# Optimization experiments

Hardware: AMD Instinct MI355X
Metric: run time of the kernel (lower is better)

## Reference

```python
import itertools
import jax, jax.numpy as jnp
import numpy as np

B, N, D = 128, 1024, 256
G, GSZ, REL_DIM, KD, PD, NF = 64, 3, 16, 64, 64, 64


def sinusoidal_pe(n, d):
    # standard transformer sinusoidal positional encoding, shape (n, d)
    pos = jnp.arange(n, dtype=jnp.float32)[:, None]
    i = jnp.arange(d, dtype=jnp.float32)[None, :]
    angle = pos / jnp.power(10000.0, (2.0 * jnp.floor(i / 2.0)) / d)
    return jnp.where(jnp.arange(d)[None, :] % 2 == 0, jnp.sin(angle), jnp.cos(angle))


def setup_inputs() -> dict:
    key = jax.random.key(0)
    k0, k1, k2, k3, k4, k5 = jax.random.split(key, 6)
    x = jax.random.normal(k0, (B, N, D), jnp.float32)
    # graphlet filter bank (random_normal init)
    filters = 0.05 * jax.random.normal(k1, (NF, GSZ, GSZ, REL_DIM), jnp.float32)
    # learned group queries: Embedding(n_groups*graphlet_size, key_dim)
    query_emb = 0.05 * jax.random.normal(k2, (G * GSZ, KD), jnp.float32)
    # Dense(key_dim, use_bias=False) for attention keys
    Wk_map = jax.random.normal(k3, (D, KD), jnp.float32) / np.sqrt(D)
    # MultiDimInnerProdRelation: per-relation-dim query/key projections
    Wq = jax.random.normal(k4, (REL_DIM, D, PD), jnp.float32) / np.sqrt(D)
    Wk = jax.random.normal(k5, (REL_DIM, D, PD), jnp.float32) / np.sqrt(D)
    return {"x": x, "filters": filters, "query_emb": query_emb,
            "Wk_map": Wk_map, "Wq": Wq, "Wk": Wk}


def reference(x, filters, query_emb, Wk_map, Wq, Wk):
    beta = KD ** (-0.5)
    # group attention: keys = Dense(x) + positional embedding ('pos+feat')
    k = jnp.einsum('bnd,dk->bnk', x, Wk_map) + sinusoidal_pe(N, KD)[None]
    scores = jax.nn.softmax(beta * jnp.einsum('qk,bnk->bqn', query_emb, k), axis=-1)
    gobj = jnp.einsum('bqn,bnd->bqd', scores, x).reshape(B, G, GSZ, D)
    # MultiDimInnerProdRelation within each group: R[b,g,i,j,r] = <Wq_r x_i, Wk_r x_j>
    zq = jnp.einsum('bgnd,rdp->bgrnp', gobj, Wq)
    zk = jnp.einsum('bgmd,rdp->bgrmp', gobj, Wk)
    R = jnp.einsum('bgrnp,bgrmp->bgnmr', zq, zk)  # (B, G, GSZ, GSZ, REL_DIM)
    # symmetric relational inner product: aggregate (mean) over permutations
    perms = jnp.array(list(itertools.permutations(range(GSZ))))  # (P, GSZ)
    Rp = R[:, :, perms[:, :, None], perms[:, None, :], :]  # (B, G, P, GSZ, GSZ, REL_DIM)
    ip = jnp.einsum('bgpnmr,fnmr->bgpf', Rp, filters)
    return jnp.mean(ip, axis=2)  # (B, n_groups, n_filters)
```

## Files before the change

kernel.cpp:

```cpp
#include <hip/hip_runtime.h>
#include <math.h>

#define B_   128
#define N_   1024
#define D_   256
#define G_   64
#define GSZ_ 3
#define RD_  16
#define KD_  64
#define PD_  64
#define NF_  64
#define Q_   (G_*GSZ_)

typedef __attribute__((ext_vector_type(8))) short bf16x8;
typedef __attribute__((ext_vector_type(4))) float f32x4;

__device__ __forceinline__ unsigned short f2bf(float f) {
    unsigned int u = __float_as_uint(f);
    u += 0x7fffu + ((u >> 16) & 1u);
    return (unsigned short)(u >> 16);
}

__global__ void coef_kernel(const float* __restrict__ filters,
                            float* __restrict__ coef) {
    int flat = blockIdx.x * 256 + threadIdx.x;
    if (flat >= NF_ * RD_) return;
    int f = flat >> 4, r = flat & 15;
    const float* F = filters + f * 144 + r;
    float diag = F[0] + F[48 + 16] + F[96 + 32];
    float all = 0.f;
#pragma unroll
    for (int u = 0; u < 3; ++u)
#pragma unroll
        for (int v = 0; v < 3; ++v) all += F[u * 48 + v * 16];
    float a = diag * (1.f / 3.f);
    float b = (all - diag) * (1.f / 6.f);
    coef[f * 16 + r] = a - b;
    coef[1024 + f * 16 + r] = b;
}

__global__ void wb_kernel(const float* __restrict__ Wq,
                          const float* __restrict__ Wk,
                          unsigned short* __restrict__ Wb) {
    int flat = blockIdx.x * 256 + threadIdx.x;
    int d = flat & 255, col = flat >> 8;
    int ch = col & 1023;
    const float* W = (col >> 10) ? Wk : Wq;
    float v = W[((size_t)(ch >> 6) * 256 + d) * 64 + (ch & 63)];
    Wb[(size_t)col * 256 + d] = f2bf(v);
}

__global__ void qeb_kernel(const float* __restrict__ qe,
                           unsigned short* __restrict__ qeb) {
    int i = blockIdx.x * 256 + threadIdx.x;
    if (i < Q_ * KD_) qeb[i] = f2bf(qe[i] * 0.125f);
}

__global__ void wkt_kernel(const float* __restrict__ Wk_map,
                           unsigned short* __restrict__ WkTb) {
    int i = blockIdx.x * 256 + threadIdx.x;
    int kd = i >> 8, d = i & 255;
    WkTb[kd * 256 + d] = f2bf(Wk_map[d * 64 + kd]);
}

__global__ __launch_bounds__(256)
void xt_kernel(const float* __restrict__ x,
               unsigned short* __restrict__ xTb) {
    __shared__ float xs[128][65];
    int b = blockIdx.z, d0 = blockIdx.y * 64, n0 = blockIdx.x * 128;
    int t = threadIdx.x;
#pragma unroll
    for (int i = 0; i < 8; ++i) {
        int f = i * 256 + t;
        int row = f >> 4, c4 = f & 15;
        float4 v = *(const float4*)(x + ((size_t)b * N_ + n0 + row) * D_ + d0 + c4 * 4);
        xs[row][c4 * 4 + 0] = v.x; xs[row][c4 * 4 + 1] = v.y;
        xs[row][c4 * 4 + 2] = v.z; xs[row][c4 * 4 + 3] = v.w;
    }
    __syncthreads();
#pragma unroll
    for (int i = 0; i < 4; ++i) {
        int f = i * 256 + t;
        int dr = f >> 4, seg = f & 15;
        uint4 uv;
        unsigned int* up = (unsigned int*)&uv;
#pragma unroll
        for (int j = 0; j < 4; ++j) {
            unsigned int lo = f2bf(xs[seg * 8 + 2 * j][dr]);
            unsigned int hi = f2bf(xs[seg * 8 + 2 * j + 1][dr]);
            up[j] = lo | (hi << 16);
        }
        *(uint4*)(xTb + ((size_t)b * D_ + d0 + dr) * N_ + n0 + seg * 8) = uv;
    }
}

#define WKP 264

__global__ __launch_bounds__(256, 2)
void kproj2_kernel(const float* __restrict__ x,
                   const unsigned short* __restrict__ WkTb,
                   unsigned short* __restrict__ kb) {
    __shared__ unsigned short wkts[64 * WKP];
    __shared__ unsigned short xs[64 * WKP];
    __shared__ unsigned short Ks[64 * 72];
    int b = blockIdx.y, n0 = blockIdx.x * 64;
    int t = threadIdx.x, w = t >> 6, lane = t & 63;
    int quad = lane >> 4, lcol = lane & 15;

#pragma unroll
    for (int i = 0; i < 8; ++i) {
        int f = i * 256 + t;
        int row = f >> 5, seg = f & 31;
        *(uint4*)(&wkts[row * WKP + seg * 8]) = *(const uint4*)(WkTb + row * 256 + seg * 8);
    }
#pragma unroll
    for (int i = 0; i < 16; ++i) {
        int f = i * 256 + t;
        int row = f >> 6, c4 = f & 63;
        float4 v = *(const float4*)(x + ((size_t)b * N_ + n0 + row) * D_ + c4 * 4);
        uint2 uv;
        uv.x = (unsigned int)f2bf(v.x) | ((unsigned int)f2bf(v.y) << 16);
        uv.y = (unsigned int)f2bf(v.z) | ((unsigned int)f2bf(v.w) << 16);
        *(uint2*)(&xs[row * WKP + c4 * 4]) = uv;
    }
    __syncthreads();

    f32x4 z[4];
#pragma unroll
    for (int mt = 0; mt < 4; ++mt) z[mt] = (f32x4)(0.f);
#pragma unroll
    for (int kk = 0; kk < 8; ++kk) {
        bf16x8 bf = *(const bf16x8*)(&xs[(w * 16 + lcol) * WKP + kk * 32 + quad * 8]);
#pragma unroll
        for (int mt = 0; mt < 4; ++mt) {
            bf16x8 af = *(const bf16x8*)(&wkts[(mt * 16 + lcol) * WKP + kk * 32 + quad * 8]);
            z[mt] = __builtin_amdgcn_mfma_f32_16x16x32_bf16(af, bf, z[mt], 0, 0, 0);
        }
    }

    int nl = w * 16 + lcol;
    int n = n0 + nl;
#pragma unroll
    for (int mt = 0; mt < 4; ++mt)
#pragma unroll
        for (int r = 0; r < 4; ++r) {
            int kd = mt * 16 + quad * 4 + r;
            float freq  = expf(-(float)(kd >> 1) * (logf(10000.0f) / 32.0f));
            float angle = (float)n * freq;
            float pe    = (kd & 1) ? cosf(angle) : sinf(angle);
            Ks[nl * 72 + kd] = f2bf(z[mt][r] + pe);
        }
    __syncthreads();

#pragma unroll
    for (int i = 0; i < 2; ++i) {
        int f = i * 256 + t;
        int row = f >> 3, seg = f & 7;
        *(uint4*)(kb + ((size_t)b * N_ + n0 + row) * KD_ + seg * 8) =
            *(const uint4*)(&Ks[row * 72 + seg * 8]);
    }
}

#define KBP 72
#define XTP 72
#define PSP 72

__global__ __launch_bounds__(256, 2)
void attn2_kernel(const unsigned short* __restrict__ qeb,
                  const unsigned short* __restrict__ kb,
                  const unsigned short* __restrict__ xTb,
                  unsigned short* __restrict__ gobj) {
    __shared__ unsigned short kbs[64 * KBP];
    __shared__ unsigned short xts[256 * XTP];
    __shared__ unsigned short ps [96 * PSP];
    __shared__ float Rs[96][4];
    __shared__ float invs[96];

    int b = blockIdx.x >> 1, qh = blockIdx.x & 1;
    int t = threadIdx.x, w = t >> 6, lane = t & 63;
    int quad = lane >> 4, lcol = lane & 15;
    int q0 = qh * 96;

    bf16x8 qef[6][2];
#pragma unroll
    for (int mt = 0; mt < 6; ++mt)
#pragma unroll
        for (int ks = 0; ks < 2; ++ks)
            qef[mt][ks] = *(const bf16x8*)(qeb + (q0 + mt * 16 + lcol) * KD_ + ks * 32 + quad * 8);

    f32x4 acc[4][6];
#pragma unroll
    for (int i = 0; i < 4; ++i)
#pragma unroll
        for (int mt = 0; mt < 6; ++mt) acc[i][mt] = (f32x4)(0.f);
    float rsum[6][4];
#pragma unroll
    for (int mt = 0; mt < 6; ++mt)
#pragma unroll
        for (int r = 0; r < 4; ++r) rsum[mt][r] = 0.f;

    const unsigned short* kbB = kb + (size_t)b * N_ * KD_;
    const unsigned short* xtB = xTb + (size_t)b * D_ * N_;

    for (int c = 0; c < 16; ++c) {
        __syncthreads();
#pragma unroll
        for (int i = 0; i < 2; ++i) {
            int flat = i * 256 + t;
            int row = flat >> 3, seg = flat & 7;
            *(uint4*)(kbs + row * KBP + seg * 8) =
                *(const uint4*)(kbB + (size_t)(c * 64 + row) * KD_ + seg * 8);
        }
#pragma unroll
        for (int i = 0; i < 8; ++i) {
            int flat = i * 256 + t;
            int row = flat >> 3, seg = flat & 7;
            *(uint4*)(xts + row * XTP + seg * 8) =
                *(const uint4*)(xtB + (size_t)row * N_ + c * 64 + seg * 8);
        }
        __syncthreads();

        f32x4 s[6];
#pragma unroll
        for (int mt = 0; mt < 6; ++mt) s[mt] = (f32x4)(0.f);
#pragma unroll
        for (int ks = 0; ks < 2; ++ks) {
            bf16x8 bf = *(const bf16x8*)(kbs + (w * 16 + lcol) * KBP + ks * 32 + quad * 8);
#pragma unroll
            for (int mt = 0; mt < 6; ++mt)
                s[mt] = __builtin_amdgcn_mfma_f32_16x16x32_bf16(qef[mt][ks], bf, s[mt], 0, 0, 0);
        }
#pragma unroll
        for (int mt = 0; mt < 6; ++mt)
#pragma unroll
            for (int r = 0; r < 4; ++r) {
                float e = __expf(s[mt][r]);
                rsum[mt][r] += e;
                ps[(mt * 16 + quad * 4 + r) * PSP + w * 16 + lcol] = f2bf(e);
            }
        __syncthreads();

#pragma unroll
        for (int ks = 0; ks < 2; ++ks) {
            bf16x8 af[6];
#pragma unroll
            for (int mt = 0; mt < 6; ++mt)
                af[mt] = *(const bf16x8*)(ps + (mt * 16 + lcol) * PSP + ks * 32 + quad * 8);
#pragma unroll
            for (int i = 0; i < 4; ++i) {
                int dt = i * 4 + w;
                bf16x8 bf = *(const bf16x8*)(xts + (dt * 16 + lcol) * XTP + ks * 32 + quad * 8);
#pragma unroll
                for (int mt = 0; mt < 6; ++mt)
                    acc[i][mt] = __builtin_amdgcn_mfma_f32_16x16x32_bf16(af[mt], bf, acc[i][mt], 0, 0, 0);
            }
        }
    }

#pragma unroll
    for (int mt = 0; mt < 6; ++mt)
#pragma unroll
        for (int r = 0; r < 4; ++r) {
            float v = rsum[mt][r];
            v += __shfl_xor(v, 1, 64);
            v += __shfl_xor(v, 2, 64);
            v += __shfl_xor(v, 4, 64);
            v += __shfl_xor(v, 8, 64);
            rsum[mt][r] = v;
        }
    if (lcol == 0) {
#pragma unroll
        for (int mt = 0; mt < 6; ++mt)
#pragma unroll
            for (int r = 0; r < 4; ++r)
                Rs[mt * 16 + quad * 4 + r][w] = rsum[mt][r];
    }
    __syncthreads();
    if (t < 96) invs[t] = 1.0f / (Rs[t][0] + Rs[t][1] + Rs[t][2] + Rs[t][3]);
    __syncthreads();

    unsigned short* gB = gobj + ((size_t)b * Q_ + q0) * D_;
#pragma unroll
    for (int i = 0; i < 4; ++i) {
        int dt = i * 4 + w;
#pragma unroll
        for (int mt = 0; mt < 6; ++mt)
#pragma unroll
            for (int r = 0; r < 4; ++r) {
                int q = mt * 16 + quad * 4 + r;
                gB[q * D_ + dt * 16 + lcol] = f2bf(acc[i][mt][r] * invs[q]);
            }
    }
}

#define APITCH 264

__global__ __launch_bounds__(256, 2)
void rel2_kernel(const unsigned short* __restrict__ gobj,
                 const unsigned short* __restrict__ Wb,
                 const float* __restrict__ coef,
                 float* __restrict__ out) {
    __shared__ unsigned short As[64 * APITCH];
    __shared__ unsigned short Ws[64 * APITCH];
    __shared__ float Tp[4 * 16 * 2 * 16];

    int t = threadIdx.x;
    int w = t >> 6, lane = t & 63;
    int quad = lane >> 4, lcol = lane & 15;
    int bg0 = blockIdx.x * 16;

    for (int i = 0; i < 8; ++i) {
        int idx = i * 256 + t;
        int r3 = idx >> 7, c3 = idx & 127;
        ((unsigned int*)As)[(r3 * 4 + 3) * (APITCH / 2) + c3] = 0u;
    }
#pragma unroll
    for (int it = 0; it < 6; ++it) {
        int flat = it * 256 + t;
        int j = flat >> 5, seg = flat & 31;
        *(uint4*)(&As[((j / 3) * 4 + (j % 3)) * APITCH + seg * 8]) =
            *(const uint4*)(gobj + ((size_t)(bg0 * 3 + j)) * D_ + seg * 8);
    }

    f32x4 zq[4], zk[4];
    for (int r = 0; r < 16; ++r) {
#pragma unroll
        for (int half = 0; half < 2; ++half) {
            __syncthreads();
            const unsigned short* src = Wb + (size_t)(r + half * 16) * 64 * 256;
#pragma unroll
            for (int it = 0; it < 8; ++it) {
                int flat = it * 256 + t;
                int col = flat >> 5, ch = flat & 31;
                uint4 v = *(const uint4*)(src + col * 256 + ch * 8);
                *(uint4*)(&Ws[col * APITCH + ch * 8]) = v;
            }
            __syncthreads();

            f32x4* z = half ? zk : zq;
#pragma unroll
            for (int i = 0; i < 4; ++i) z[i] = (f32x4)(0.f);
#pragma unroll
            for (int kk = 0; kk < 8; ++kk) {
                bf16x8 bfrag = *(const bf16x8*)(&Ws[(w * 16 + lcol) * APITCH + kk * 32 + quad * 8]);
#pragma unroll
                for (int mt = 0; mt < 4; ++mt) {
                    bf16x8 afrag = *(const bf16x8*)(&As[(mt * 16 + lcol) * APITCH + kk * 32 + quad * 8]);
                    z[mt] = __builtin_amdgcn_mfma_f32_16x16x32_bf16(afrag, bfrag, z[mt], 0, 0, 0);
                }
            }
        }
#pragma unroll
        for (int mt = 0; mt < 4; ++mt) {
            float t1 = zq[mt].x * zk[mt].x + zq[mt].y * zk[mt].y +
                       zq[mt].z * zk[mt].z + zq[mt].w * zk[mt].w;
            float sq = zq[mt].x + zq[mt].y + zq[mt].z + zq[mt].w;
            float sk = zk[mt].x + zk[mt].y + zk[mt].z + zk[mt].w;
            float t2 = sq * sk;
#pragma unroll
            for (int off = 1; off < 16; off <<= 1) {
                t1 += __shfl_xor(t1, off, 64);
                t2 += __shfl_xor(t2, off, 64);
            }
            if (lcol == 0) {
                int bgl = mt * 4 + quad;
                Tp[((w * 16 + bgl) * 2 + 0) * 16 + r] = t1;
                Tp[((w * 16 + bgl) * 2 + 1) * 16 + r] = t2;
            }
        }
    }
    __syncthreads();

    int f = t & 63;
#pragma unroll
    for (int i = 0; i < 4; ++i) {
        int bgl = w * 4 + i;
        float acc = 0.f;
#pragma unroll
        for (int r = 0; r < 16; ++r) {
            float T1 = Tp[((0 * 16 + bgl) * 2 + 0) * 16 + r] + Tp[((1 * 16 + bgl) * 2 + 0) * 16 + r] +
                       Tp[((2 * 16 + bgl) * 2 + 0) * 16 + r] + Tp[((3 * 16 + bgl) * 2 + 0) * 16 + r];
            float T2 = Tp[((0 * 16 + bgl) * 2 + 1) * 16 + r] + Tp[((1 * 16 + bgl) * 2 + 1) * 16 + r] +
                       Tp[((2 * 16 + bgl) * 2 + 1) * 16 + r] + Tp[((3 * 16 + bgl) * 2 + 1) * 16 + r];
            acc += coef[f * 16 + r] * T1 + coef[1024 + f * 16 + r] * T2;
        }
        out[(size_t)(bg0 + bgl) * NF_ + f] = acc;
    }
}

extern "C" void kernel_launch(void* const* d_in, const int* in_sizes, int n_in,
                              void* d_out, int out_size, void* d_ws, size_t ws_size,
                              hipStream_t stream) {
    const float* x         = (const float*)d_in[0];
    const float* filters   = (const float*)d_in[1];
    const float* query_emb = (const float*)d_in[2];
    const float* Wk_map    = (const float*)d_in[3];
    const float* Wq        = (const float*)d_in[4];
    const float* Wk        = (const float*)d_in[5];
    float* out = (float*)d_out;

    char* p = (char*)d_ws;
    unsigned short* xTb  = (unsigned short*)p;  p += (size_t)B_*D_*N_*2;
    unsigned short* kbp  = (unsigned short*)p;  p += (size_t)B_*N_*KD_*2;
    unsigned short* gobj = (unsigned short*)p;  p += (size_t)B_*Q_*D_*2;
    unsigned short* Wb   = (unsigned short*)p;  p += (size_t)2048*256*2;
    float*          coef = (float*)p;           p += 2048*4;
    unsigned short* qeb  = (unsigned short*)p;  p += (size_t)Q_*KD_*2;
    unsigned short* WkTb = (unsigned short*)p;  p += (size_t)KD_*D_*2;

    hipLaunchKernelGGL(wkt_kernel, dim3(64), dim3(256), 0, stream,
                       Wk_map, WkTb);
    hipLaunchKernelGGL(xt_kernel, dim3(8, 4, 128), dim3(256), 0, stream,
                       x, xTb);
    hipLaunchKernelGGL(kproj2_kernel, dim3(16, 128), dim3(256), 0, stream,
                       x, WkTb, kbp);
    hipLaunchKernelGGL(qeb_kernel, dim3(48), dim3(256), 0, stream,
                       query_emb, qeb);
    hipLaunchKernelGGL(coef_kernel, dim3(4), dim3(256), 0, stream,
                       filters, coef);
    hipLaunchKernelGGL(wb_kernel, dim3(2048), dim3(256), 0, stream,
                       Wq, Wk, Wb);
    hipLaunchKernelGGL(attn2_kernel, dim3(256), dim3(256), 0, stream,
                       qeb, kbp, xTb, gobj);
    hipLaunchKernelGGL(rel2_kernel, dim3(512), dim3(256), 0, stream,
                       gobj, Wb, coef, out);
}
```

Baseline: 401.6 us.

## Load MFMA operands directly from global memory in attention and relation kernels

The attention kernel no longer stages key and transposed-x tiles in shared memory. Each wave reads its MFMA B fragments straight from global memory, which removes the staging copies and one barrier pair per chunk, at the cost of uncoalesced, cache-dependent loads. The relation kernel now handles 32 groups per block with half the grid. It processes two relation dims at a time, for both q and k, and reads the W fragments directly from global memory instead of through a shared Ws buffer. This cuts the syncthreads per relation dim, but raises register pressure and global traffic per block.

```diff
diff --git a/kernel.cpp b/kernel.cpp
--- a/kernel.cpp
+++ b/kernel.cpp
@@ -161,18 +161,14 @@
     }
 }
 
-#define KBP 72
-#define XTP 72
 #define PSP 72
 
 __global__ __launch_bounds__(256, 2)
-void attn2_kernel(const unsigned short* __restrict__ qeb,
+void attn3_kernel(const unsigned short* __restrict__ qeb,
                   const unsigned short* __restrict__ kb,
                   const unsigned short* __restrict__ xTb,
                   unsigned short* __restrict__ gobj) {
-    __shared__ unsigned short kbs[64 * KBP];
-    __shared__ unsigned short xts[256 * XTP];
-    __shared__ unsigned short ps [96 * PSP];
+    __shared__ unsigned short ps[96 * PSP];
     __shared__ float Rs[96][4];
     __shared__ float invs[96];
 
@@ -203,29 +199,12 @@
     const unsigned short* xtB = xTb + (size_t)b * D_ * N_;
 
     for (int c = 0; c < 16; ++c) {
-        __syncthreads();
-#pragma unroll
-        for (int i = 0; i < 2; ++i) {
-            int flat = i * 256 + t;
-            int row = flat >> 3, seg = flat & 7;
-            *(uint4*)(kbs + row * KBP + seg * 8) =
-                *(const uint4*)(kbB + (size_t)(c * 64 + row) * KD_ + seg * 8);
-        }
-#pragma unroll
-        for (int i = 0; i < 8; ++i) {
-            int flat = i * 256 + t;
-            int row = flat >> 3, seg = flat & 7;
-            *(uint4*)(xts + row * XTP + seg * 8) =
-                *(const uint4*)(xtB + (size_t)row * N_ + c * 64 + seg * 8);
-        }
-        __syncthreads();
-
         f32x4 s[6];
 #pragma unroll
         for (int mt = 0; mt < 6; ++mt) s[mt] = (f32x4)(0.f);
 #pragma unroll
         for (int ks = 0; ks < 2; ++ks) {
-            bf16x8 bf = *(const bf16x8*)(kbs + (w * 16 + lcol) * KBP + ks * 32 + quad * 8);
+            bf16x8 bf = *(const bf16x8*)(kbB + (size_t)(c * 64 + w * 16 + lcol) * KD_ + ks * 32 + quad * 8);
 #pragma unroll
             for (int mt = 0; mt < 6; ++mt)
                 s[mt] = __builtin_amdgcn_mfma_f32_16x16x32_bf16(qef[mt][ks], bf, s[mt], 0, 0, 0);
@@ -235,10 +214,16 @@
 #pragma unroll
             for (int r = 0; r < 4; ++r) {
                 float e = __expf(s[mt][r]);
+                s[mt][r] = e;
                 rsum[mt][r] += e;
-                ps[(mt * 16 + quad * 4 + r) * PSP + w * 16 + lcol] = f2bf(e);
             }
         __syncthreads();
+#pragma unroll
+        for (int mt = 0; mt < 6; ++mt)
+#pragma unroll
+            for (int r = 0; r < 4; ++r)
+                ps[(mt * 16 + quad * 4 + r) * PSP + w * 16 + lcol] = f2bf(s[mt][r]);
+        __syncthreads();
 
 #pragma unroll
         for (int ks = 0; ks < 2; ++ks) {
@@ -249,7 +234,7 @@
 #pragma unroll
             for (int i = 0; i < 4; ++i) {
                 int dt = i * 4 + w;
-                bf16x8 bf = *(const bf16x8*)(xts + (dt * 16 + lcol) * XTP + ks * 32 + quad * 8);
+                bf16x8 bf = *(const bf16x8*)(xtB + (size_t)(dt * 16 + lcol) * N_ + c * 64 + ks * 32 + quad * 8);
 #pragma unroll
                 for (int mt = 0; mt < 6; ++mt)
                     acc[i][mt] = __builtin_amdgcn_mfma_f32_16x16x32_bf16(af[mt], bf, acc[i][mt], 0, 0, 0);
@@ -293,98 +278,110 @@
     }
 }
 
-#define APITCH 264
+#define AP3 264
 
 __global__ __launch_bounds__(256, 2)
-void rel2_kernel(const unsigned short* __restrict__ gobj,
+void rel3_kernel(const unsigned short* __restrict__ gobj,
                  const unsigned short* __restrict__ Wb,
                  const float* __restrict__ coef,
                  float* __restrict__ out) {
-    __shared__ unsigned short As[64 * APITCH];
-    __shared__ unsigned short Ws[64 * APITCH];
-    __shared__ float Tp[4 * 16 * 2 * 16];
-
-    int t = threadIdx.x;
-    int w = t >> 6, lane = t & 63;
+    __shared__ unsigned short As[128 * AP3];
+    __shared__ float Tp[4096];
+
+    int t = threadIdx.x, w = t >> 6, lane = t & 63;
     int quad = lane >> 4, lcol = lane & 15;
-    int bg0 = blockIdx.x * 16;
-
-    for (int i = 0; i < 8; ++i) {
+    int bg0 = blockIdx.x * 32;
+    int pcol = w * 16 + lcol;
+
+#pragma unroll
+    for (int i = 0; i < 4; ++i) {
         int idx = i * 256 + t;
-        int r3 = idx >> 7, c3 = idx & 127;
-        ((unsigned int*)As)[(r3 * 4 + 3) * (APITCH / 2) + c3] = 0u;
-    }
-#pragma unroll
-    for (int it = 0; it < 6; ++it) {
-        int flat = it * 256 + t;
-        int j = flat >> 5, seg = flat & 31;
-        *(uint4*)(&As[((j / 3) * 4 + (j % 3)) * APITCH + seg * 8]) =
-            *(const uint4*)(gobj + ((size_t)(bg0 * 3 + j)) * D_ + seg * 8);
-    }
-
-    f32x4 zq[4], zk[4];
-    for (int r = 0; r < 16; ++r) {
-#pragma unroll
-        for (int half = 0; half < 2; ++half) {
-            __syncthreads();
-            const unsigned short* src = Wb + (size_t)(r + half * 16) * 64 * 256;
-#pragma unroll
-            for (int it = 0; it < 8; ++it) {
-                int flat = it * 256 + t;
-                int col = flat >> 5, ch = flat & 31;
-                uint4 v = *(const uint4*)(src + col * 256 + ch * 8);
-                *(uint4*)(&Ws[col * APITCH + ch * 8]) = v;
+        int r3 = idx >> 5, c4 = idx & 31;
+        uint4 zz; zz.x = zz.y = zz.z = zz.w = 0u;
+        *(uint4*)(&As[(r3 * 4 + 3) * AP3 + c4 * 8]) = zz;
+    }
+#pragma unroll
+    for (int i = 0; i < 12; ++i) {
+        int idx = i * 256 + t;
+        int j = idx >> 5, c4 = idx & 31;
+        *(uint4*)(&As[((j / 3) * 4 + (j % 3)) * AP3 + c4 * 8]) =
+            *(const uint4*)(gobj + ((size_t)(bg0 * 3 + j)) * 256 + c4 * 8);
+    }
+    __syncthreads();
+
+    for (int rp = 0; rp < 8; ++rp) {
+        f32x4 zq0[8], zq1[8], zk0[8], zk1[8];
+#pragma unroll
+        for (int mt = 0; mt < 8; ++mt) {
+            zq0[mt] = (f32x4)(0.f); zq1[mt] = (f32x4)(0.f);
+            zk0[mt] = (f32x4)(0.f); zk1[mt] = (f32x4)(0.f);
+        }
+        const unsigned short* bq0p = Wb + (size_t)((2 * rp) * 64 + pcol) * 256;
+        const unsigned short* bq1p = Wb + (size_t)((2 * rp + 1) * 64 + pcol) * 256;
+        const unsigned short* bk0p = bq0p + (size_t)1024 * 256;
+        const unsigned short* bk1p = bq1p + (size_t)1024 * 256;
+#pragma unroll
+        for (int kk = 0; kk < 8; ++kk) {
+            int co = kk * 32 + quad * 8;
+            bf16x8 bq0 = *(const bf16x8*)(bq0p + co);
+            bf16x8 bk0 = *(const bf16x8*)(bk0p + co);
+            bf16x8 bq1 = *(const bf16x8*)(bq1p + co);
+            bf16x8 bk1 = *(const bf16x8*)(bk1p + co);
+#pragma unroll
+            for (int mt = 0; mt < 8; ++mt) {
+                bf16x8 af = *(const bf16x8*)(&As[(mt * 16 + lcol) * AP3 + co]);
+                zq0[mt] = __builtin_amdgcn_mfma_f32_16x16x32_bf16(af, bq0, zq0[mt], 0, 0, 0);
+                zk0[mt] = __builtin_amdgcn_mfma_f32_16x16x32_bf16(af, bk0, zk0[mt], 0, 0, 0);
+                zq1[mt] = __builtin_amdgcn_mfma_f32_16x16x32_bf16(af, bq1, zq1[mt], 0, 0, 0);
+                zk1[mt] = __builtin_amdgcn_mfma_f32_16x16x32_bf16(af, bk1, zk1[mt], 0, 0, 0);
             }
-            __syncthreads();
-
-            f32x4* z = half ? zk : zq;
-#pragma unroll
-            for (int i = 0; i < 4; ++i) z[i] = (f32x4)(0.f);
-#pragma unroll
-            for (int kk = 0; kk < 8; ++kk) {
-                bf16x8 bfrag = *(const bf16x8*)(&Ws[(w * 16 + lcol) * APITCH + kk * 32 + quad * 8]);
-#pragma unroll
-                for (int mt = 0; mt < 4; ++mt) {
-                    bf16x8 afrag = *(const bf16x8*)(&As[(mt * 16 + lcol) * APITCH + kk * 32 + quad * 8]);
-                    z[mt] = __builtin_amdgcn_mfma_f32_16x16x32_bf16(afrag, bfrag, z[mt], 0, 0, 0);
+        }
+#pragma unroll
+        for (int rr = 0; rr < 2; ++rr) {
+            int r = 2 * rp + rr;
+#pragma unroll
+            for (int mt = 0; mt < 8; ++mt) {
+                f32x4 zq = rr ? zq1[mt] : zq0[mt];
+                f32x4 zk = rr ? zk1[mt] : zk0[mt];
+                float t1 = zq.x * zk.x + zq.y * zk.y + zq.z * zk.z + zq.w * zk.w;
+                float sq = zq.x + zq.y + zq.z + zq.w;
+                float sk = zk.x + zk.y + zk.z + zk.w;
+                float t2 = sq * sk;
+#pragma unroll
+                for (int off = 1; off < 16; off <<= 1) {
+                    t1 += __shfl_xor(t1, off, 64);
+                    t2 += __shfl_xor(t2, off, 64);
+                }
+                if (lcol == 0) {
+                    int bgl = mt * 4 + quad;
+                    Tp[((w * 32 + bgl) * 2 + 0) * 16 + r] = t1;
+                    Tp[((w * 32 + bgl) * 2 + 1) * 16 + r] = t2;
                 }
             }
         }
-#pragma unroll
-        for (int mt = 0; mt < 4; ++mt) {
-            float t1 = zq[mt].x * zk[mt].x + zq[mt].y * zk[mt].y +
-                       zq[mt].z * zk[mt].z + zq[mt].w * zk[mt].w;
-            float sq = zq[mt].x + zq[mt].y + zq[mt].z + zq[mt].w;
-            float sk = zk[mt].x + zk[mt].y + zk[mt].z + zk[mt].w;
-            float t2 = sq * sk;
-#pragma unroll
-            for (int off = 1; off < 16; off <<= 1) {
-                t1 += __shfl_xor(t1, off, 64);
-                t2 += __shfl_xor(t2, off, 64);
-            }
-            if (lcol == 0) {
-                int bgl = mt * 4 + quad;
-                Tp[((w * 16 + bgl) * 2 + 0) * 16 + r] = t1;
-                Tp[((w * 16 + bgl) * 2 + 1) * 16 + r] = t2;
-            }
-        }
-    }
-    __syncthreads();
-
-    int f = t & 63;
-#pragma unroll
-    for (int i = 0; i < 4; ++i) {
-        int bgl = w * 4 + i;
-        float acc = 0.f;
+    }
+    __syncthreads();
+
+    int f = t & 63, g8 = t >> 6;
+    float c1v[16], c2v[16];
+#pragma unroll
+    for (int r = 0; r < 16; ++r) {
+        c1v[r] = coef[f * 16 + r];
+        c2v[r] = coef[1024 + f * 16 + r];
+    }
+#pragma unroll
+    for (int i = 0; i < 8; ++i) {
+        int bgl = g8 * 8 + i;
+        float a = 0.f;
 #pragma unroll
         for (int r = 0; r < 16; ++r) {
-            float T1 = Tp[((0 * 16 + bgl) * 2 + 0) * 16 + r] + Tp[((1 * 16 + bgl) * 2 + 0) * 16 + r] +
-                       Tp[((2 * 16 + bgl) * 2 + 0) * 16 + r] + Tp[((3 * 16 + bgl) * 2 + 0) * 16 + r];
-            float T2 = Tp[((0 * 16 + bgl) * 2 + 1) * 16 + r] + Tp[((1 * 16 + bgl) * 2 + 1) * 16 + r] +
-                       Tp[((2 * 16 + bgl) * 2 + 1) * 16 + r] + Tp[((3 * 16 + bgl) * 2 + 1) * 16 + r];
-            acc += coef[f * 16 + r] * T1 + coef[1024 + f * 16 + r] * T2;
-        }
-        out[(size_t)(bg0 + bgl) * NF_ + f] = acc;
+            float T1 = Tp[((0 * 32 + bgl) * 2 + 0) * 16 + r] + Tp[((1 * 32 + bgl) * 2 + 0) * 16 + r] +
+                       Tp[((2 * 32 + bgl) * 2 + 0) * 16 + r] + Tp[((3 * 32 + bgl) * 2 + 0) * 16 + r];
+            float T2 = Tp[((0 * 32 + bgl) * 2 + 1) * 16 + r] + Tp[((1 * 32 + bgl) * 2 + 1) * 16 + r] +
+                       Tp[((2 * 32 + bgl) * 2 + 1) * 16 + r] + Tp[((3 * 32 + bgl) * 2 + 1) * 16 + r];
+            a += c1v[r] * T1 + c2v[r] * T2;
+        }
+        out[(size_t)(bg0 + bgl) * NF_ + f] = a;
     }
 }
 
@@ -420,8 +417,8 @@
                        filters, coef);
     hipLaunchKernelGGL(wb_kernel, dim3(2048), dim3(256), 0, stream,
                        Wq, Wk, Wb);
-    hipLaunchKernelGGL(attn2_kernel, dim3(256), dim3(256), 0, stream,
+    hipLaunchKernelGGL(attn3_kernel, dim3(256), dim3(256), 0, stream,
                        qeb, kbp, xTb, gobj);
-    hipLaunchKernelGGL(rel2_kernel, dim3(512), dim3(256), 0, stream,
+    hipLaunchKernelGGL(rel3_kernel, dim3(256), dim3(256), 0, stream,
                        gobj, Wb, coef, out);
 }
```

Result: no change. 399.7 us (-0.5%).
